# Optimization experiments

Hardware: AMD Instinct MI355X
Metric: run time of the kernel (lower is better)

The kernel has to match this reference:

```python
import jax, jax.numpy as jnp
import numpy as np

B, K, D, H = 16384, 3, 1024, 16
DH = D // H  # head_dim = 64


def setup_inputs() -> dict:
    key = jax.random.key(0)
    ks = jax.random.split(key, 12)
    s = 1.0 / np.sqrt(D)
    inp = {
        "tokens": jax.random.normal(ks[0], (B, K, D), dtype=jnp.float32),
        "ctx": jax.random.normal(ks[1], (B, 1, D), dtype=jnp.float32),
        "Wq": jax.random.uniform(ks[2], (D, D), jnp.float32, -s, s),
        "bq": jnp.zeros((D,), jnp.float32),
        "Wk": jax.random.uniform(ks[3], (D, D), jnp.float32, -s, s),
        "bk": jnp.zeros((D,), jnp.float32),
        "Wv": jax.random.uniform(ks[4], (D, D), jnp.float32, -s, s),
        "bv": jnp.zeros((D,), jnp.float32),
        "Wc": jax.random.uniform(ks[5], (D, D), jnp.float32, -s, s),
        "bc": jnp.zeros((D,), jnp.float32),
        "Wo": jax.random.uniform(ks[6], (D, D), jnp.float32, -s, s),
        "bo": jnp.zeros((D,), jnp.float32),
    }
    return inp


def _split_heads(x):
    # (B, L, D) -> (B, H, L, DH)
    Bq, L, _ = x.shape
    return x.reshape(Bq, L, H, DH).transpose(0, 2, 1, 3)


def reference(tokens, ctx, Wq, bq, Wk, bk, Wv, bv, Wc, bc, Wo, bo):
    q = _split_heads(tokens @ Wq.T + bq)          # (B,H,K,DH)
    k = _split_heads(tokens @ Wk.T + bk)          # (B,H,K,DH)
    v = _split_heads(tokens @ Wv.T + bv)          # (B,H,K,DH)
    c = _split_heads(ctx @ Wc.T + bc)             # (B,H,1,DH)
    k_ctx = k * c                                  # context-modulated keys
    v_ctx = v * c                                  # context-modulated values
    scores = jnp.einsum("bhqd,bhkd->bhqk", q, k_ctx) / jnp.sqrt(jnp.float32(DH))
    probs = jax.nn.softmax(scores, axis=-1)       # dropout p=0.0 -> identity
    out = jnp.einsum("bhqk,bhkd->bhqd", probs, v_ctx)
    out = out.transpose(0, 2, 1, 3).reshape(tokens.shape[0], K, D)  # merge heads
    return out @ Wo.T + bo
```

## Files before the change

### kernel.cpp

```cpp
#include <hip/hip_runtime.h>
#include <hip/hip_bf16.h>

#define BB 16384
#define KK 3
#define DD 1024
#define HH 16

typedef __attribute__((ext_vector_type(8))) short bf16x8;
typedef __attribute__((ext_vector_type(4))) float f32x4;
typedef unsigned int u32;

__device__ __forceinline__ void load_lds16(const void* g, void* l) {
  __builtin_amdgcn_global_load_lds(
      (const __attribute__((address_space(1))) u32*)g,
      (__attribute__((address_space(3))) u32*)l,
      16, 0, 0);
}

__device__ __forceinline__ unsigned short f2bf(float f) {
  __hip_bfloat16 h = __float2bfloat16(f);
  unsigned short u;
  __builtin_memcpy(&u, &h, 2);
  return u;
}

__device__ __forceinline__ float bf2f(unsigned short u) {
  union { float f; u32 i; } cv;
  cv.i = ((u32)u) << 16;
  return cv.f;
}

__global__ void cast_f32_bf16(const float* __restrict__ in,
                              unsigned short* __restrict__ out, int n4) {
  int stride = gridDim.x * blockDim.x;
  for (int i = blockIdx.x * blockDim.x + threadIdx.x; i < n4; i += stride) {
    float4 v = ((const float4*)in)[i];
    ushort4 o;
    o.x = f2bf(v.x);
    o.y = f2bf(v.y);
    o.z = f2bf(v.z);
    o.w = f2bf(v.w);
    ((ushort4*)out)[i] = o;
  }
}

template <bool OUT_F32>
__global__ __launch_bounds__(512, 2)
void gemm256(const __hip_bfloat16* __restrict__ A,
             const __hip_bfloat16* __restrict__ Bt,
             const float* __restrict__ bias,
             void* __restrict__ Cout,
             int M, int N, int K) {
  __shared__ __align__(128) char lds[131072];

  const int nTn = N >> 8;
  const int nwg = (M >> 8) * nTn;
  int bid = blockIdx.x;
  bid = (bid & 7) * (nwg >> 3) + (bid >> 3);
  const int tm = bid / nTn;
  const int tn = bid % nTn;

  const int tid = threadIdx.x;
  const int l = tid & 63;
  const int w = tid >> 6;
  const int wm = w >> 2;
  const int wn = w & 3;
  const int l15 = l & 15;
  const int g = l >> 4;
  const int l7 = l15 & 7;

  const int aBase = (l15 << 7) + (((wm << 2) + g) ^ l7) * 16;
  const int bBase = 16384 + ((((wn & 1) << 6) + l15) << 7) +
                    ((((wn >> 1) << 2) + g) ^ l7) * 16;

  const size_t strideK = (size_t)K * 2;
  const char* Ab = (const char*)A + (size_t)tm * 256 * strideK;
  const char* Bb = (const char*)Bt + (size_t)tn * 256 * strideK;
  const int q = (tid & 7) ^ ((tid >> 3) & 7);
  const size_t g0 = (size_t)((q >> 2) * 128 + (tid >> 3)) * strideK + (q & 3) * 16;
  const size_t g1 = g0 + (size_t)64 * strideK;
  const int sld = tid << 4;

  f32x4 acc[8][4] = {};
  const int nkt = K >> 5;

#define STAGE_A(T)                                                        \
  {                                                                       \
    char* sb = lds + (((T) & 3) << 15);                                   \
    const char* ga = Ab + ((size_t)(T) << 6);                             \
    load_lds16(ga + g0, sb + sld);                                        \
    load_lds16(ga + g1, sb + 8192 + sld);                                 \
  }
#define STAGE_B(T)                                                        \
  {                                                                       \
    char* sb = lds + (((T) & 3) << 15);                                   \
    const char* gb = Bb + ((size_t)(T) << 6);                             \
    load_lds16(gb + g0, sb + 16384 + sld);                                \
    load_lds16(gb + g1, sb + 24576 + sld);                                \
  }
#define MFMA_HALF(H)                                                      \
  __builtin_amdgcn_s_setprio(1);                                          \
  _Pragma("unroll") for (int mm = 0; mm < 4; ++mm)                        \
      _Pragma("unroll") for (int nn = 0; nn < 4; ++nn)                    \
          acc[(H) + mm][nn] = __builtin_amdgcn_mfma_f32_16x16x32_bf16(    \
              af[mm], bfr[nn], acc[(H) + mm][nn], 0, 0, 0);               \
  __builtin_amdgcn_s_setprio(0);

  STAGE_A(0); STAGE_B(0);
  STAGE_A(1); STAGE_B(1);
  STAGE_A(2); STAGE_B(2);
  asm volatile("s_waitcnt vmcnt(8)" ::: "memory");
  __builtin_amdgcn_s_barrier();

  for (int kt = 0; kt < nkt; ++kt) {
    const char* slot = lds + ((kt & 3) << 15);
    bf16x8 af[4], bfr[4];

#pragma unroll
    for (int n = 0; n < 4; ++n)
      bfr[n] = *(const bf16x8*)(slot + bBase + (n << 11));
#pragma unroll
    for (int m = 0; m < 4; ++m)
      af[m] = *(const bf16x8*)(slot + aBase + (m << 11));
    if (kt + 3 < nkt) STAGE_A(kt + 3);
    __builtin_amdgcn_s_barrier();
    asm volatile("s_waitcnt lgkmcnt(0)" ::: "memory");
    MFMA_HALF(0)
    __builtin_amdgcn_s_barrier();

#pragma unroll
    for (int m = 0; m < 4; ++m)
      af[m] = *(const bf16x8*)(slot + aBase + ((m + 4) << 11));
    if (kt + 3 < nkt) STAGE_B(kt + 3);
    if (kt < nkt - 3)
      asm volatile("s_waitcnt vmcnt(8)" ::: "memory");
    else if (kt == nkt - 3)
      asm volatile("s_waitcnt vmcnt(4)" ::: "memory");
    else if (kt == nkt - 2)
      asm volatile("s_waitcnt vmcnt(0)" ::: "memory");
    __builtin_amdgcn_s_barrier();
    asm volatile("s_waitcnt lgkmcnt(0)" ::: "memory");
    MFMA_HALF(4)
    __builtin_amdgcn_s_barrier();
  }
#undef STAGE_A
#undef STAGE_B
#undef MFMA_HALF

  const int cbase = tn * 256 + (wn << 6) + l15;
  float b4[4];
#pragma unroll
  for (int n = 0; n < 4; ++n) b4[n] = bias[cbase + (n << 4)];
  const size_t rbase = (size_t)tm * 256 + (wm << 7) + ((l >> 4) << 2);
#pragma unroll
  for (int m = 0; m < 8; ++m) {
#pragma unroll
    for (int j = 0; j < 4; ++j) {
      const size_t row = rbase + (m << 4) + j;
#pragma unroll
      for (int n = 0; n < 4; ++n) {
        const int col = cbase + (n << 4);
        float v = acc[m][n][j] + b4[n];
        if (OUT_F32)
          ((float*)Cout)[row * N + col] = v;
        else
          ((unsigned short*)Cout)[row * N + col] = f2bf(v);
      }
    }
  }
}

__global__ __launch_bounds__(256)
void attn_kernel(const unsigned short* __restrict__ QKV,
                 const unsigned short* __restrict__ Cp,
                 unsigned short* __restrict__ Out) {
  const int t = threadIdx.x;
  const int grp = (blockIdx.x << 4) + (t >> 4);
  const int x = t & 15;
  const int b = grp >> 4;
  const int h = grp & 15;

  const size_t col = (size_t)h * 64 + (x << 2);
  const size_t qbase = (size_t)b * 3 * 3072 + col;

  ushort4 cu = *(const ushort4*)&Cp[(size_t)b * 1024 + col];
  float c[4] = {bf2f(cu.x), bf2f(cu.y), bf2f(cu.z), bf2f(cu.w)};

  float q[3][4], kc[3][4], vc[3][4];
#pragma unroll
  for (int i = 0; i < 3; ++i) {
    ushort4 qu = *(const ushort4*)&QKV[qbase + (size_t)i * 3072];
    ushort4 ku = *(const ushort4*)&QKV[qbase + (size_t)i * 3072 + 1024];
    ushort4 vu = *(const ushort4*)&QKV[qbase + (size_t)i * 3072 + 2048];
    q[i][0] = bf2f(qu.x); q[i][1] = bf2f(qu.y); q[i][2] = bf2f(qu.z); q[i][3] = bf2f(qu.w);
    kc[i][0] = bf2f(ku.x) * c[0]; kc[i][1] = bf2f(ku.y) * c[1];
    kc[i][2] = bf2f(ku.z) * c[2]; kc[i][3] = bf2f(ku.w) * c[3];
    vc[i][0] = bf2f(vu.x) * c[0]; vc[i][1] = bf2f(vu.y) * c[1];
    vc[i][2] = bf2f(vu.z) * c[2]; vc[i][3] = bf2f(vu.w) * c[3];
  }

  float s[9];
#pragma unroll
  for (int i = 0; i < 3; ++i)
#pragma unroll
    for (int j = 0; j < 3; ++j)
      s[i * 3 + j] = q[i][0] * kc[j][0] + q[i][1] * kc[j][1] +
                     q[i][2] * kc[j][2] + q[i][3] * kc[j][3];

#pragma unroll
  for (int off = 8; off > 0; off >>= 1)
#pragma unroll
    for (int e = 0; e < 9; ++e)
      s[e] += __shfl_xor(s[e], off, 64);

  const float scale = 0.125f;
#pragma unroll
  for (int i = 0; i < 3; ++i) {
    float s0 = s[i * 3 + 0] * scale;
    float s1 = s[i * 3 + 1] * scale;
    float s2 = s[i * 3 + 2] * scale;
    float m = fmaxf(fmaxf(s0, s1), s2);
    float p0 = expf(s0 - m), p1 = expf(s1 - m), p2 = expf(s2 - m);
    float inv = 1.0f / (p0 + p1 + p2);
    ushort4 o;
    o.x = f2bf((p0 * vc[0][0] + p1 * vc[1][0] + p2 * vc[2][0]) * inv);
    o.y = f2bf((p0 * vc[0][1] + p1 * vc[1][1] + p2 * vc[2][1]) * inv);
    o.z = f2bf((p0 * vc[0][2] + p1 * vc[1][2] + p2 * vc[2][2]) * inv);
    o.w = f2bf((p0 * vc[0][3] + p1 * vc[1][3] + p2 * vc[2][3]) * inv);
    *(ushort4*)&Out[(size_t)(b * 3 + i) * 1024 + col] = o;
  }
}

extern "C" void kernel_launch(void* const* d_in, const int* in_sizes, int n_in,
                              void* d_out, int out_size, void* d_ws, size_t ws_size,
                              hipStream_t stream) {
  const float* tokens = (const float*)d_in[0];
  const float* ctx    = (const float*)d_in[1];
  const float* Wq     = (const float*)d_in[2];
  const float* bq     = (const float*)d_in[3];
  const float* Wk     = (const float*)d_in[4];
  const float* bk     = (const float*)d_in[5];
  const float* Wv     = (const float*)d_in[6];
  const float* bv     = (const float*)d_in[7];
  const float* Wc     = (const float*)d_in[8];
  const float* bc     = (const float*)d_in[9];
  const float* Wo     = (const float*)d_in[10];
  const float* bo     = (const float*)d_in[11];

  const int M  = BB * KK;
  const int Mc = BB;
  const int D  = DD;

  char* p = (char*)d_ws;
  auto carve = [&](size_t bytes) {
    char* r = p;
    p += (bytes + 255) & ~(size_t)255;
    return r;
  };
  unsigned short* Xb   = (unsigned short*)carve((size_t)M * D * 2);
  unsigned short* Cin  = (unsigned short*)carve((size_t)Mc * D * 2);
  unsigned short* Wqkv = (unsigned short*)carve((size_t)3 * D * D * 2);
  unsigned short* Wcb  = (unsigned short*)carve((size_t)D * D * 2);
  unsigned short* Wob  = (unsigned short*)carve((size_t)D * D * 2);
  float*          bqkv = (float*)carve((size_t)3 * D * 4);
  unsigned short* QKV  = (unsigned short*)carve((size_t)M * 3 * D * 2);
  unsigned short* Cpr  = (unsigned short*)carve((size_t)Mc * D * 2);

  hipLaunchKernelGGL(cast_f32_bf16, dim3(4096), dim3(256), 0, stream, tokens, Xb, M * D / 4);
  hipLaunchKernelGGL(cast_f32_bf16, dim3(2048), dim3(256), 0, stream, ctx, Cin, Mc * D / 4);
  hipLaunchKernelGGL(cast_f32_bf16, dim3(512), dim3(256), 0, stream, Wq, Wqkv, D * D / 4);
  hipLaunchKernelGGL(cast_f32_bf16, dim3(512), dim3(256), 0, stream, Wk, Wqkv + D * D, D * D / 4);
  hipLaunchKernelGGL(cast_f32_bf16, dim3(512), dim3(256), 0, stream, Wv, Wqkv + 2 * D * D, D * D / 4);
  hipLaunchKernelGGL(cast_f32_bf16, dim3(512), dim3(256), 0, stream, Wc, Wcb, D * D / 4);
  hipLaunchKernelGGL(cast_f32_bf16, dim3(512), dim3(256), 0, stream, Wo, Wob, D * D / 4);
  hipMemcpyAsync(bqkv, bq, D * 4, hipMemcpyDeviceToDevice, stream);
  hipMemcpyAsync(bqkv + D, bk, D * 4, hipMemcpyDeviceToDevice, stream);
  hipMemcpyAsync(bqkv + 2 * D, bv, D * 4, hipMemcpyDeviceToDevice, stream);

  hipLaunchKernelGGL((gemm256<false>), dim3((M / 256) * (3 * D / 256)), dim3(512), 0, stream,
                     (const __hip_bfloat16*)Xb, (const __hip_bfloat16*)Wqkv, bqkv,
                     (void*)QKV, M, 3 * D, D);
  hipLaunchKernelGGL((gemm256<false>), dim3((Mc / 256) * (D / 256)), dim3(512), 0, stream,
                     (const __hip_bfloat16*)Cin, (const __hip_bfloat16*)Wcb, bc,
                     (void*)Cpr, Mc, D, D);
  hipLaunchKernelGGL(attn_kernel, dim3(BB * HH / 16), dim3(256), 0, stream, QKV, Cpr, Xb);
  hipLaunchKernelGGL((gemm256<true>), dim3((M / 256) * (D / 256)), dim3(512), 0, stream,
                     (const __hip_bfloat16*)Xb, (const __hip_bfloat16*)Wob, bo,
                     d_out, M, D, D);
}
```

Measured before the change: 666.4 us.

## Restructure GEMM main loop with B-fragment register double-buffering and fewer barriers

```diff
diff --git a/kernel.cpp b/kernel.cpp
--- a/kernel.cpp
+++ b/kernel.cpp
@@ -84,67 +84,70 @@
   f32x4 acc[8][4] = {};
   const int nkt = K >> 5;
 
-#define STAGE_A(T)                                                        \
+#define STAGE_AB(T)                                                       \
   {                                                                       \
     char* sb = lds + (((T) & 3) << 15);                                   \
     const char* ga = Ab + ((size_t)(T) << 6);                             \
+    const char* gb = Bb + ((size_t)(T) << 6);                             \
     load_lds16(ga + g0, sb + sld);                                        \
     load_lds16(ga + g1, sb + 8192 + sld);                                 \
-  }
-#define STAGE_B(T)                                                        \
-  {                                                                       \
-    char* sb = lds + (((T) & 3) << 15);                                   \
-    const char* gb = Bb + ((size_t)(T) << 6);                             \
     load_lds16(gb + g0, sb + 16384 + sld);                                \
     load_lds16(gb + g1, sb + 24576 + sld);                                \
   }
-#define MFMA_HALF(H)                                                      \
+
+#define MFMA_HALF(H, BF)                                                  \
   __builtin_amdgcn_s_setprio(1);                                          \
   _Pragma("unroll") for (int mm = 0; mm < 4; ++mm)                        \
       _Pragma("unroll") for (int nn = 0; nn < 4; ++nn)                    \
           acc[(H) + mm][nn] = __builtin_amdgcn_mfma_f32_16x16x32_bf16(    \
-              af[mm], bfr[nn], acc[(H) + mm][nn], 0, 0, 0);               \
+              a8[(H) + mm], BF[nn], acc[(H) + mm][nn], 0, 0, 0);          \
   __builtin_amdgcn_s_setprio(0);
 
-  STAGE_A(0); STAGE_B(0);
-  STAGE_A(1); STAGE_B(1);
-  STAGE_A(2); STAGE_B(2);
+#define TILE(KT, Bc, Bn)                                                  \
+  {                                                                       \
+    const int kt_ = (KT);                                                 \
+    const char* slot = lds + ((kt_ & 3) << 15);                           \
+    bf16x8 a8[8];                                                         \
+    _Pragma("unroll") for (int mm = 0; mm < 8; ++mm)                      \
+        a8[mm] = *(const bf16x8*)(slot + aBase + (mm << 11));             \
+    if (kt_ + 3 < nkt) STAGE_AB(kt_ + 3);                                 \
+    if (kt_ < nkt - 3)                                                    \
+      asm volatile("s_waitcnt vmcnt(8)" ::: "memory");                    \
+    else if (kt_ == nkt - 3)                                              \
+      asm volatile("s_waitcnt vmcnt(4)" ::: "memory");                    \
+    else if (kt_ == nkt - 2)                                              \
+      asm volatile("s_waitcnt vmcnt(0)" ::: "memory");                    \
+    __builtin_amdgcn_s_barrier();                                         \
+    asm volatile("" ::: "memory");                                        \
+    if (kt_ + 1 < nkt) {                                                  \
+      const char* sn = lds + (((kt_ + 1) & 3) << 15);                     \
+      _Pragma("unroll") for (int nn = 0; nn < 4; ++nn)                    \
+          Bn[nn] = *(const bf16x8*)(sn + bBase + (nn << 11));             \
+    }                                                                     \
+    MFMA_HALF(0, Bc)                                                      \
+    MFMA_HALF(4, Bc)                                                      \
+    __builtin_amdgcn_s_barrier();                                         \
+    asm volatile("" ::: "memory");                                        \
+  }
+
+  STAGE_AB(0);
+  STAGE_AB(1);
+  STAGE_AB(2);
   asm volatile("s_waitcnt vmcnt(8)" ::: "memory");
   __builtin_amdgcn_s_barrier();
-
-  for (int kt = 0; kt < nkt; ++kt) {
-    const char* slot = lds + ((kt & 3) << 15);
-    bf16x8 af[4], bfr[4];
-
-#pragma unroll
-    for (int n = 0; n < 4; ++n)
-      bfr[n] = *(const bf16x8*)(slot + bBase + (n << 11));
-#pragma unroll
-    for (int m = 0; m < 4; ++m)
-      af[m] = *(const bf16x8*)(slot + aBase + (m << 11));
-    if (kt + 3 < nkt) STAGE_A(kt + 3);
-    __builtin_amdgcn_s_barrier();
-    asm volatile("s_waitcnt lgkmcnt(0)" ::: "memory");
-    MFMA_HALF(0)
-    __builtin_amdgcn_s_barrier();
-
-#pragma unroll
-    for (int m = 0; m < 4; ++m)
-      af[m] = *(const bf16x8*)(slot + aBase + ((m + 4) << 11));
-    if (kt + 3 < nkt) STAGE_B(kt + 3);
-    if (kt < nkt - 3)
-      asm volatile("s_waitcnt vmcnt(8)" ::: "memory");
-    else if (kt == nkt - 3)
-      asm volatile("s_waitcnt vmcnt(4)" ::: "memory");
-    else if (kt == nkt - 2)
-      asm volatile("s_waitcnt vmcnt(0)" ::: "memory");
-    __builtin_amdgcn_s_barrier();
-    asm volatile("s_waitcnt lgkmcnt(0)" ::: "memory");
-    MFMA_HALF(4)
-    __builtin_amdgcn_s_barrier();
-  }
-#undef STAGE_A
-#undef STAGE_B
+  asm volatile("" ::: "memory");
+
+  bf16x8 bX[4], bY[4];
+#pragma unroll
+  for (int nn = 0; nn < 4; ++nn)
+    bX[nn] = *(const bf16x8*)(lds + bBase + (nn << 11));
+
+  for (int kt = 0; kt < nkt; kt += 2) {
+    TILE(kt, bX, bY)
+    TILE(kt + 1, bY, bX)
+  }
+#undef TILE
+#undef STAGE_AB
 #undef MFMA_HALF
 
   const int cbase = tn * 256 + (wn << 6) + l15;
```

Measured after the change: 698.6 us. 4.8% more time.

## Restructure GEMM main loop to one barrier per K-tile with merged A/B staging

Applied to the files above, without the earlier changes.

```diff
diff --git a/kernel.cpp b/kernel.cpp
--- a/kernel.cpp
+++ b/kernel.cpp
@@ -84,68 +84,52 @@
   f32x4 acc[8][4] = {};
   const int nkt = K >> 5;
 
-#define STAGE_A(T)                                                        \
+#define STAGE_AB(T)                                                       \
   {                                                                       \
     char* sb = lds + (((T) & 3) << 15);                                   \
     const char* ga = Ab + ((size_t)(T) << 6);                             \
+    const char* gb = Bb + ((size_t)(T) << 6);                             \
     load_lds16(ga + g0, sb + sld);                                        \
     load_lds16(ga + g1, sb + 8192 + sld);                                 \
-  }
-#define STAGE_B(T)                                                        \
-  {                                                                       \
-    char* sb = lds + (((T) & 3) << 15);                                   \
-    const char* gb = Bb + ((size_t)(T) << 6);                             \
     load_lds16(gb + g0, sb + 16384 + sld);                                \
     load_lds16(gb + g1, sb + 24576 + sld);                                \
   }
-#define MFMA_HALF(H)                                                      \
-  __builtin_amdgcn_s_setprio(1);                                          \
-  _Pragma("unroll") for (int mm = 0; mm < 4; ++mm)                        \
-      _Pragma("unroll") for (int nn = 0; nn < 4; ++nn)                    \
-          acc[(H) + mm][nn] = __builtin_amdgcn_mfma_f32_16x16x32_bf16(    \
-              af[mm], bfr[nn], acc[(H) + mm][nn], 0, 0, 0);               \
-  __builtin_amdgcn_s_setprio(0);
-
-  STAGE_A(0); STAGE_B(0);
-  STAGE_A(1); STAGE_B(1);
-  STAGE_A(2); STAGE_B(2);
-  asm volatile("s_waitcnt vmcnt(8)" ::: "memory");
-  __builtin_amdgcn_s_barrier();
+
+  STAGE_AB(0);
+  STAGE_AB(1);
+  STAGE_AB(2);
 
   for (int kt = 0; kt < nkt; ++kt) {
+    if (kt <= nkt - 3)
+      asm volatile("s_waitcnt vmcnt(8)" ::: "memory");
+    else if (kt == nkt - 2)
+      asm volatile("s_waitcnt vmcnt(4)" ::: "memory");
+    else
+      asm volatile("s_waitcnt vmcnt(0)" ::: "memory");
+    __builtin_amdgcn_s_barrier();
+    asm volatile("" ::: "memory");
+
     const char* slot = lds + ((kt & 3) << 15);
-    bf16x8 af[4], bfr[4];
-
+    bf16x8 bfr[4], af[8];
 #pragma unroll
     for (int n = 0; n < 4; ++n)
       bfr[n] = *(const bf16x8*)(slot + bBase + (n << 11));
 #pragma unroll
-    for (int m = 0; m < 4; ++m)
+    for (int m = 0; m < 8; ++m)
       af[m] = *(const bf16x8*)(slot + aBase + (m << 11));
-    if (kt + 3 < nkt) STAGE_A(kt + 3);
-    __builtin_amdgcn_s_barrier();
-    asm volatile("s_waitcnt lgkmcnt(0)" ::: "memory");
-    MFMA_HALF(0)
-    __builtin_amdgcn_s_barrier();
-
-#pragma unroll
-    for (int m = 0; m < 4; ++m)
-      af[m] = *(const bf16x8*)(slot + aBase + ((m + 4) << 11));
-    if (kt + 3 < nkt) STAGE_B(kt + 3);
-    if (kt < nkt - 3)
-      asm volatile("s_waitcnt vmcnt(8)" ::: "memory");
-    else if (kt == nkt - 3)
-      asm volatile("s_waitcnt vmcnt(4)" ::: "memory");
-    else if (kt == nkt - 2)
-      asm volatile("s_waitcnt vmcnt(0)" ::: "memory");
-    __builtin_amdgcn_s_barrier();
-    asm volatile("s_waitcnt lgkmcnt(0)" ::: "memory");
-    MFMA_HALF(4)
-    __builtin_amdgcn_s_barrier();
-  }
-#undef STAGE_A
-#undef STAGE_B
-#undef MFMA_HALF
+
+    if (kt + 3 < nkt) STAGE_AB(kt + 3);
+
+    __builtin_amdgcn_s_setprio(1);
+#pragma unroll
+    for (int m = 0; m < 8; ++m)
+#pragma unroll
+      for (int n = 0; n < 4; ++n)
+        acc[m][n] = __builtin_amdgcn_mfma_f32_16x16x32_bf16(af[m], bfr[n],
+                                                            acc[m][n], 0, 0, 0);
+    __builtin_amdgcn_s_setprio(0);
+  }
+#undef STAGE_AB
 
   const int cbase = tn * 256 + (wn << 6) + l15;
   float b4[4];
```

Result: no change. 656.5 us (-1.5%).
